# Kernel tuning notes

Measured on AMD Instinct MI355X. Metric: run time of the kernel, lower is better.

The kernel has to match this reference:

```python
import jax, jax.numpy as jnp
import numpy as np

K = 3
PAD = 1
DIL = 1
EPS = 1e-5


def _conv2d(x, w, b=None, pad=1):
    y = jax.lax.conv_general_dilated(x, w, (1, 1), [(pad, pad), (pad, pad)],
                                     dimension_numbers=('NCHW', 'OIHW', 'NCHW'))
    if b is not None:
        y = y + b[None, :, None, None]
    return y


def _conv_transpose(x, w, stride=2, pad=1):
    # torch ConvTranspose2d(k=4, s=2, p=1): lhs-dilated conv with flipped, transposed kernel
    kh = w.shape[2]
    w_t = jnp.flip(w, (2, 3)).transpose(1, 0, 2, 3)  # [in,out,kh,kw] -> [out,in,kh,kw]
    p = kh - 1 - pad
    return jax.lax.conv_general_dilated(x, w_t, (1, 1), [(p, p), (p, p)],
                                        lhs_dilation=(stride, stride),
                                        dimension_numbers=('NCHW', 'OIHW', 'NCHW'))


def _bn(x, g, b):
    # BatchNorm2d training-mode forward (batch stats, biased var)
    m = x.mean(axis=(0, 2, 3), keepdims=True)
    v = x.var(axis=(0, 2, 3), keepdims=True)
    return (x - m) * jax.lax.rsqrt(v + EPS) * g[None, :, None, None] + b[None, :, None, None]


def _deform_conv(x, off_x, off_y, mask, w):
    # Modulated deformable conv v2, stride=1, pad=K//2, groups=1, deform_groups=1
    B, C, H, W = x.shape
    K2 = K * K
    ky, kx = jnp.meshgrid(jnp.arange(K), jnp.arange(K), indexing='ij')
    base_y = (ky.reshape(-1) * DIL - PAD).astype(x.dtype)  # [K2]
    base_x = (kx.reshape(-1) * DIL - PAD).astype(x.dtype)
    hh = jnp.arange(H, dtype=x.dtype)
    ww = jnp.arange(W, dtype=x.dtype)
    # sampling coords per kernel tap: [B, K2, H, W]
    sy = off_y + base_y[None, :, None, None] + hh[None, None, :, None]
    sx = off_x + base_x[None, :, None, None] + ww[None, None, None, :]
    y0 = jnp.floor(sy)
    x0 = jnp.floor(sx)
    ly = sy - y0
    lx = sx - x0
    xf = x.reshape(B, C, H * W)

    def corner(yi, xi, wgt):
        valid = ((yi >= 0) & (yi < H) & (xi >= 0) & (xi < W)).astype(x.dtype)
        idx = (jnp.clip(yi, 0, H - 1) * W + jnp.clip(xi, 0, W - 1)).astype(jnp.int32)
        idx = idx.reshape(B, K2, H * W)
        v = jnp.take_along_axis(xf[:, :, None, :], idx[:, None, :, :], axis=3)  # [B,C,K2,HW]
        return v * (wgt * valid).reshape(B, 1, K2, H * W)

    val = (corner(y0, x0, (1 - ly) * (1 - lx)) + corner(y0, x0 + 1, (1 - ly) * lx)
           + corner(y0 + 1, x0, ly * (1 - lx)) + corner(y0 + 1, x0 + 1, ly * lx))
    val = val * mask.reshape(B, 1, K2, H * W)  # modulation
    O = w.shape[0]
    out = jnp.einsum('bip,oi->bop', val.reshape(B, C * K2, H * W), w.reshape(O, C * K2))
    return out.reshape(B, O, H, W)


def setup_inputs() -> dict:
    key = jax.random.key(0)
    ks = jax.random.split(key, 6)
    B, C, H, W, O = 4, 256, 64, 64, 256
    x = jax.random.normal(ks[0], (B, C, H, W), jnp.float32)
    w_off = jax.random.normal(ks[1], (3 * K * K, C, K, K), jnp.float32) * 0.01
    b_off = jax.random.normal(ks[2], (3 * K * K,), jnp.float32) * 0.01
    w_dcn = jax.random.normal(ks[3], (O, C, K, K), jnp.float32) * float(np.sqrt(2.0 / (C * K * K)))
    w_up = jax.random.normal(ks[4], (O, O, 4, 4), jnp.float32) * 0.02
    gamma1 = jnp.ones((O,), jnp.float32)
    beta1 = jnp.zeros((O,), jnp.float32)
    gamma2 = jnp.ones((O,), jnp.float32)
    beta2 = jnp.zeros((O,), jnp.float32)
    return dict(x=x, w_off=w_off, b_off=b_off, w_dcn=w_dcn, gamma1=gamma1, beta1=beta1,
                w_up=w_up, gamma2=gamma2, beta2=beta2)


def reference(x, w_off, b_off, w_dcn, gamma1, beta1, w_up, gamma2, beta2):
    offset_mask = _conv2d(x, w_off, b_off, pad=K // 2)
    off_x, off_y, mask = jnp.split(offset_mask, 3, axis=1)
    mask = jax.nn.sigmoid(mask)
    y = _deform_conv(x, off_x, off_y, mask, w_dcn)
    y = jax.nn.relu(_bn(y, gamma1, beta1))
    y_up = _conv_transpose(y, w_up)
    y_up = jax.nn.relu(_bn(y_up, gamma2, beta2))
    return (y, y_up)
```

## Files before the change

kernel.cpp:

```cpp
#include <hip/hip_runtime.h>
#include <math.h>

#define BB 4
#define CC 256
#define OC 256
#define HH 64
#define WW2 64
#define HW 4096
#define UP_HW 16384
#define NOFF 27
#define EPSV 1e-5f
#define TPX 32

typedef _Float16 f16;
typedef f16 f16x2 __attribute__((ext_vector_type(2)));
typedef f16 f16x4 __attribute__((ext_vector_type(4)));
typedef f16 f16x8 __attribute__((ext_vector_type(8)));
typedef float f32x4 __attribute__((ext_vector_type(4)));

#define GLOAD16(GP, LP) __builtin_amdgcn_global_load_lds( \
    (const __attribute__((address_space(1))) void*)(GP),  \
    (__attribute__((address_space(3))) void*)(LP), 16, 0, 0)

__global__ __launch_bounds__(256) void k_offset(
    const float* __restrict__ x, const float* __restrict__ w,
    const float* __restrict__ bias, float* __restrict__ om) {
  const int b = blockIdx.z;
  const int ocg = blockIdx.y * 3;
  const int row = threadIdx.x >> 6;
  const int h = blockIdx.x * 4 + row;
  const int col = threadIdx.x & 63;
  const float* xb = x + (size_t)b * CC * HW;
  float a0 = 0.f, a1 = 0.f, a2 = 0.f;
  for (int ic = 0; ic < CC; ++ic) {
    const float* xc = xb + ic * HW;
    float xm[3], xl[3], xr[3];
    #pragma unroll
    for (int dy = 0; dy < 3; ++dy) {
      int hy = h + dy - 1;
      float v = (hy >= 0 && hy < HH) ? xc[hy * WW2 + col] : 0.f;
      xm[dy] = v;
      float up = __shfl_up(v, 1, 64);
      float dn = __shfl_down(v, 1, 64);
      xl[dy] = (col == 0) ? 0.f : up;
      xr[dy] = (col == 63) ? 0.f : dn;
    }
    #pragma unroll
    for (int j = 0; j < 3; ++j) {
      const float* wp = w + ((size_t)(ocg + j) * CC + ic) * 9;
      float s = 0.f;
      #pragma unroll
      for (int dy = 0; dy < 3; ++dy) {
        s = fmaf(wp[dy * 3 + 0], xl[dy], s);
        s = fmaf(wp[dy * 3 + 1], xm[dy], s);
        s = fmaf(wp[dy * 3 + 2], xr[dy], s);
      }
      if (j == 0) a0 += s; else if (j == 1) a1 += s; else a2 += s;
    }
  }
  #pragma unroll
  for (int j = 0; j < 3; ++j) {
    int oc = ocg + j;
    float v = (j == 0 ? a0 : (j == 1 ? a1 : a2)) + bias[oc];
    if (oc >= 18) v = 1.f / (1.f + expf(-v));
    om[((size_t)(b * NOFF + oc)) * HW + h * WW2 + col] = v;
  }
}

__global__ __launch_bounds__(256) void k_dcn(
    const float* __restrict__ x, const float* __restrict__ om,
    const float* __restrict__ wd, float* __restrict__ out) {
  __shared__ int s_idx[4][TPX * 9];
  __shared__ float s_bw[4][TPX * 9];
  __shared__ __align__(16) float s_v[2][TPX * 9];
  __shared__ __align__(16) float s_wd[2][9][256];
  const int b = blockIdx.y;
  const int p0 = blockIdx.x * TPX;
  const int h = p0 >> 6;
  const int tid = threadIdx.x;

  for (int e = tid; e < TPX * 9; e += 256) {
    int px = e & (TPX - 1);
    int k = e >> 5;
    int p = p0 + px;
    int wc = p & 63;
    float offx = om[((size_t)(b * NOFF + k)) * HW + p];
    float offy = om[((size_t)(b * NOFF + 9 + k)) * HW + p];
    float msk  = om[((size_t)(b * NOFF + 18 + k)) * HW + p];
    float sy = offy + (float)(k / 3 - 1) + (float)h;
    float sx = offx + (float)(k % 3 - 1) + (float)wc;
    float fy = floorf(sy), fx = floorf(sx);
    float ly = sy - fy, lx = sx - fx;
    int iy = (int)fy, ix = (int)fx;
    #pragma unroll
    for (int cnr = 0; cnr < 4; ++cnr) {
      int dy = cnr >> 1, dx = cnr & 1;
      int yy = iy + dy, xx = ix + dx;
      bool val = (yy >= 0) & (yy < HH) & (xx >= 0) & (xx < WW2);
      float wt = (dy ? ly : 1.f - ly) * (dx ? lx : 1.f - lx) * msk;
      s_idx[cnr][e] = val ? (yy * WW2 + xx) : 0;
      s_bw[cnr][e] = val ? wt : 0.f;
    }
  }
  __syncthreads();

  const int og = tid >> 3, pg = tid & 7;
  float acc[8][4] = {};
  const float* xb = x + (size_t)b * CC * HW;
  for (int ic = 0; ic < CC; ic += 2) {
    {
      const float* wp = wd + (size_t)tid * (CC * 9) + ic * 9;
      #pragma unroll
      for (int t = 0; t < 18; ++t)
        s_wd[t / 9][t % 9][tid] = wp[t];
    }
    #pragma unroll
    for (int t = 0; t < 3; ++t) {
      int e = tid + t * 256;
      if (e < 2 * TPX * 9) {
        int icc = (e >= TPX * 9);
        int r = e - icc * TPX * 9;
        const float* xc = xb + (ic + icc) * HW;
        float v = s_bw[0][r] * xc[s_idx[0][r]] + s_bw[1][r] * xc[s_idx[1][r]]
                + s_bw[2][r] * xc[s_idx[2][r]] + s_bw[3][r] * xc[s_idx[3][r]];
        s_v[icc][r] = v;
      }
    }
    __syncthreads();
    #pragma unroll
    for (int icc = 0; icc < 2; ++icc) {
      #pragma unroll
      for (int k = 0; k < 9; ++k) {
        float4 v4 = *(const float4*)&s_v[icc][k * TPX + pg * 4];
        float4 wa = *(const float4*)&s_wd[icc][k][og * 8];
        float4 wb = *(const float4*)&s_wd[icc][k][og * 8 + 4];
        float vi[4] = {v4.x, v4.y, v4.z, v4.w};
        float wj[8] = {wa.x, wa.y, wa.z, wa.w, wb.x, wb.y, wb.z, wb.w};
        #pragma unroll
        for (int j = 0; j < 8; ++j)
          #pragma unroll
          for (int i = 0; i < 4; ++i)
            acc[j][i] = fmaf(wj[j], vi[i], acc[j][i]);
      }
    }
    __syncthreads();
  }
  #pragma unroll
  for (int j = 0; j < 8; ++j) {
    int oc = og * 8 + j;
    float4 o = make_float4(acc[j][0], acc[j][1], acc[j][2], acc[j][3]);
    *(float4*)&out[((size_t)(b * OC + oc)) * HW + p0 + pg * 4] = o;
  }
}

__global__ __launch_bounds__(256) void k_stats(
    const float* __restrict__ d, int perB, float* __restrict__ mean,
    float* __restrict__ rinv) {
  const int c = blockIdx.x, tid = threadIdx.x;
  double s1 = 0.0, s2 = 0.0;
  const int n4 = perB >> 2;
  for (int b = 0; b < BB; ++b) {
    const float4* p = (const float4*)(d + ((size_t)(b * CC + c)) * perB);
    for (int i = tid; i < n4; i += 256) {
      float4 v = p[i];
      s1 += (double)v.x + (double)v.y + (double)v.z + (double)v.w;
      s2 += (double)v.x * v.x + (double)v.y * v.y + (double)v.z * v.z + (double)v.w * v.w;
    }
  }
  __shared__ double r1[256], r2[256];
  r1[tid] = s1; r2[tid] = s2;
  __syncthreads();
  for (int s = 128; s > 0; s >>= 1) {
    if (tid < s) { r1[tid] += r1[tid + s]; r2[tid] += r2[tid + s]; }
    __syncthreads();
  }
  if (tid == 0) {
    double n = (double)perB * BB;
    double m = r1[0] / n;
    double var = r2[0] / n - m * m;
    mean[c] = (float)m;
    rinv[c] = (float)(1.0 / sqrt(var + (double)EPSV));
  }
}

__global__ __launch_bounds__(256) void k_stats_part(
    const float* __restrict__ d, int perB, double* __restrict__ part) {
  const int c = blockIdx.x & 255, b = blockIdx.x >> 8;
  const int tid = threadIdx.x;
  double s1 = 0.0, s2 = 0.0;
  const float4* p = (const float4*)(d + ((size_t)(b * CC + c)) * perB);
  const int n4 = perB >> 2;
  for (int i = tid; i < n4; i += 256) {
    float4 v = p[i];
    s1 += (double)v.x + (double)v.y + (double)v.z + (double)v.w;
    s2 += (double)v.x * v.x + (double)v.y * v.y + (double)v.z * v.z + (double)v.w * v.w;
  }
  __shared__ double r1[256], r2[256];
  r1[tid] = s1; r2[tid] = s2;
  __syncthreads();
  for (int s = 128; s > 0; s >>= 1) {
    if (tid < s) { r1[tid] += r1[tid + s]; r2[tid] += r2[tid + s]; }
    __syncthreads();
  }
  if (tid == 0) {
    part[blockIdx.x] = r1[0];
    part[1024 + blockIdx.x] = r2[0];
  }
}

__global__ __launch_bounds__(256) void k_stats_fin(
    const double* __restrict__ part, int perB, float* __restrict__ mean,
    float* __restrict__ rinv) {
  const int c = threadIdx.x;
  double s1 = 0.0, s2 = 0.0;
  #pragma unroll
  for (int b = 0; b < BB; ++b) {
    s1 += part[b * 256 + c];
    s2 += part[1024 + b * 256 + c];
  }
  double n = (double)perB * BB;
  double m = s1 / n;
  double var = s2 / n - m * m;
  mean[c] = (float)m;
  rinv[c] = (float)(1.0 / sqrt(var + (double)EPSV));
}

__global__ __launch_bounds__(256) void k_bnrelu(
    float* __restrict__ d, const float* __restrict__ mean,
    const float* __restrict__ rinv, const float* __restrict__ g,
    const float* __restrict__ be, int perB, int total4) {
  int stride = gridDim.x * blockDim.x;
  for (int i4 = blockIdx.x * blockDim.x + threadIdx.x; i4 < total4; i4 += stride) {
    int c = (int)((((long long)i4 * 4) / perB) & 255);
    float sc = rinv[c] * g[c];
    float shv = fmaf(-mean[c], sc, be[c]);
    float4 v = ((float4*)d)[i4];
    v.x = fmaxf(fmaf(v.x, sc, shv), 0.f);
    v.y = fmaxf(fmaf(v.y, sc, shv), 0.f);
    v.z = fmaxf(fmaf(v.z, sc, shv), 0.f);
    v.w = fmaxf(fmaf(v.w, sc, shv), 0.f);
    ((float4*)d)[i4] = v;
  }
}

__global__ __launch_bounds__(256) void k_totile(const float* __restrict__ y,
                                                f16* __restrict__ yTp) {
  __shared__ float S[32][33];
  const int h = blockIdx.x;
  const int cg = blockIdx.y >> 1;
  const int wg = blockIdx.y & 1;
  const int b = blockIdx.z;
  const int t = threadIdx.x;
  {
    int ci = t >> 3, q = t & 7;
    const float* src = y + (((size_t)(b * 256 + cg * 32 + ci) * 64 + h) * 64 + wg * 32 + q * 4);
    float4 v = *(const float4*)src;
    S[ci][q * 4 + 0] = v.x; S[ci][q * 4 + 1] = v.y;
    S[ci][q * 4 + 2] = v.z; S[ci][q * 4 + 3] = v.w;
  }
  __syncthreads();
  {
    int w = t >> 3, c2 = t & 7;
    f16x4 pv;
    pv[0] = (f16)S[c2 * 4 + 0][w];
    pv[1] = (f16)S[c2 * 4 + 1][w];
    pv[2] = (f16)S[c2 * 4 + 2][w];
    pv[3] = (f16)S[c2 * 4 + 3][w];
    f16* dst = yTp + (((size_t)(b * 66 + h + 1) * 66 + (wg * 32 + w + 1)) * 256 + cg * 32 + c2 * 4);
    *(f16x4*)dst = pv;
  }
}

__global__ __launch_bounds__(256) void k_totile_bn(
    const float* __restrict__ mean, const float* __restrict__ rinv,
    const float* __restrict__ g, const float* __restrict__ be,
    float* __restrict__ y, f16* __restrict__ yTp) {
  __shared__ float S[32][33];
  const int h = blockIdx.x;
  const int cg = blockIdx.y >> 1;
  const int wg = blockIdx.y & 1;
  const int b = blockIdx.z;
  const int t = threadIdx.x;
  {
    int ci = t >> 3, q = t & 7;
    int c = cg * 32 + ci;
    float sc = rinv[c] * g[c];
    float sh = fmaf(-mean[c], sc, be[c]);
    float* src = y + (((size_t)(b * 256 + c) * 64 + h) * 64 + wg * 32 + q * 4);
    float4 v = *(const float4*)src;
    v.x = fmaxf(fmaf(v.x, sc, sh), 0.f);
    v.y = fmaxf(fmaf(v.y, sc, sh), 0.f);
    v.z = fmaxf(fmaf(v.z, sc, sh), 0.f);
    v.w = fmaxf(fmaf(v.w, sc, sh), 0.f);
    *(float4*)src = v;
    S[ci][q * 4 + 0] = v.x; S[ci][q * 4 + 1] = v.y;
    S[ci][q * 4 + 2] = v.z; S[ci][q * 4 + 3] = v.w;
  }
  __syncthreads();
  {
    int w = t >> 3, c2 = t & 7;
    f16x4 pv;
    pv[0] = (f16)S[c2 * 4 + 0][w];
    pv[1] = (f16)S[c2 * 4 + 1][w];
    pv[2] = (f16)S[c2 * 4 + 2][w];
    pv[3] = (f16)S[c2 * 4 + 3][w];
    f16* dst = yTp + (((size_t)(b * 66 + h + 1) * 66 + (wg * 32 + w + 1)) * 256 + cg * 32 + c2 * 4);
    *(f16x4*)dst = pv;
  }
}

__global__ __launch_bounds__(128) void k_pad0(f16* __restrict__ p0,
                                              f16* __restrict__ p1) {
  f16* base = blockIdx.z ? p1 : p0;
  const int j = blockIdx.x;
  const int b = blockIdx.y;
  int row, col;
  if (j < 66)       { row = 0;      col = j; }
  else if (j < 132) { row = 65;     col = j - 66; }
  else if (j < 196) { row = j - 131; col = 0; }
  else              { row = j - 195; col = 65; }
  unsigned int* p = (unsigned int*)&base[(((size_t)b * 66 + row) * 66 + col) * 256];
  p[threadIdx.x] = 0u;
}

__global__ __launch_bounds__(256) void k_wdprep(const float* __restrict__ wd,
                                                f16* __restrict__ Wd) {
  const int oc = blockIdx.x, ic = threadIdx.x;
  const float* src = wd + ((size_t)oc * 256 + ic) * 9;
  f16* dst = Wd + (((size_t)(ic >> 3) * 256 + oc)) * 8 + (ic & 7);
  #pragma unroll
  for (int tap = 0; tap < 9; ++tap)
    dst[(size_t)tap * 32 * 256 * 8] = (f16)src[tap];
}

__global__ __launch_bounds__(256) void k_wodprep(const float* __restrict__ wo,
                                                 f16* __restrict__ Wod) {
  const int oc = blockIdx.x;
  const int ic = threadIdx.x;
  const int icg = ic >> 3, e = ic & 7;
  #pragma unroll
  for (int tap = 0; tap < 9; ++tap) {
    f16 v = (f16)0.f;
    if (oc < NOFF) v = (f16)wo[((size_t)oc * 256 + ic) * 9 + tap];
    Wod[(((size_t)(tap * 32 + icg)) * 32 + oc) * 8 + e] = v;
  }
}

__global__ __launch_bounds__(256) void k_off_mfma(
    const f16* __restrict__ xtp, const f16* __restrict__ Wod,
    const float* __restrict__ bias, float* __restrict__ om) {
  __shared__ __align__(16) f16 Alds[9 * 4 * 32 * 8];
  __shared__ __align__(16) f16 Blds[3 * 4 * 66 * 8];
  const int b = blockIdx.y;
  const int r = blockIdx.x;
  const int tid = threadIdx.x;
  const int lane = tid & 63, wave = tid >> 6;
  const int l15 = lane & 15, l4 = lane >> 4;
  const int wbase = tid & 192;
  f32x4 acc[2] = {};
  const size_t xbase = ((size_t)b * 66 + r) * 66;

  for (int ic0 = 0; ic0 < 256; ic0 += 32) {
    __syncthreads();
    #pragma unroll
    for (int i = 0; i < 5; ++i) {
      int idx = i * 256 + tid;
      if (idx < 1152) {
        int tap = idx >> 7, g = (idx >> 5) & 3, oc = idx & 31;
        const f16* gp = Wod + (((size_t)(tap * 32 + (ic0 >> 3) + g)) * 32 + oc) * 8;
        GLOAD16(gp, Alds + (size_t)(i * 256 + wbase) * 8);
      }
    }
    #pragma unroll
    for (int i = 0; i < 4; ++i) {
      int idx = i * 256 + tid;
      if (idx < 792) {
        int rp4g = idx / 66, c = idx - rp4g * 66;
        int rp = rp4g >> 2, g = rp4g & 3;
        const f16* gp = xtp + ((xbase + rp * 66 + c) * 256 + ic0 + g * 8);
        GLOAD16(gp, Blds + (size_t)(i * 256 + wbase) * 8);
      }
    }
    __syncthreads();
    #pragma unroll
    for (int tap = 0; tap < 9; ++tap) {
      const int ky = tap / 3, kx = tap % 3;
      f16x8 af[2];
      #pragma unroll
      for (int fi = 0; fi < 2; ++fi)
        af[fi] = *(const f16x8*)&Alds[((tap * 4 + l4) * 32 + fi * 16 + l15) * 8];
      f16x8 bf = *(const f16x8*)&Blds[((ky * 4 + l4) * 66 + wave * 16 + l15 + kx) * 8];
      #pragma unroll
      for (int fi = 0; fi < 2; ++fi)
        acc[fi] = __builtin_amdgcn_mfma_f32_16x16x32_f16(af[fi], bf, acc[fi], 0, 0, 0);
    }
  }
  #pragma unroll
  for (int fi = 0; fi < 2; ++fi) {
    #pragma unroll
    for (int r4 = 0; r4 < 4; ++r4) {
      int oc = fi * 16 + l4 * 4 + r4;
      if (oc < NOFF) {
        float v = acc[fi][r4] + bias[oc];
        if (oc >= 18) v = 1.f / (1.f + expf(-v));
        om[((size_t)(b * NOFF + oc)) * HW + r * 64 + wave * 16 + l15] = v;
      }
    }
  }
}

__global__ __launch_bounds__(256) void k_sample(
    const f16* __restrict__ xtp, const float* __restrict__ om,
    f16* __restrict__ V, int b0) {
  const int tap = blockIdx.y;
  const int vb = blockIdx.z;
  const int b = b0 + vb;
  const int p = blockIdx.x * 64 + (threadIdx.x & 63);
  const int icg0 = threadIdx.x >> 6;
  const int h = p >> 6, w = p & 63;
  const float offx = om[((size_t)(b * NOFF + tap)) * HW + p];
  const float offy = om[((size_t)(b * NOFF + 9 + tap)) * HW + p];
  const float msk  = om[((size_t)(b * NOFF + 18 + tap)) * HW + p];
  float sy = offy + (float)(tap / 3 - 1) + (float)h;
  float sx = offx + (float)(tap % 3 - 1) + (float)w;
  float fy = floorf(sy), fx = floorf(sx);
  float ly = sy - fy, lx = sx - fx;
  int iy = (int)fy, ix = (int)fx;
  int idx[4];
  float wg[4];
  #pragma unroll
  for (int cnr = 0; cnr < 4; ++cnr) {
    int dy = cnr >> 1, dx = cnr & 1;
    int yy = iy + dy, xx = ix + dx;
    bool val = (yy >= 0) & (yy < HH) & (xx >= 0) & (xx < WW2);
    float wt = (dy ? ly : 1.f - ly) * (dx ? lx : 1.f - lx) * msk;
    idx[cnr] = val ? ((yy + 1) * 66 + (xx + 1)) : 0;
    wg[cnr] = val ? wt : 0.f;
  }
  const f16* xb = xtp + (size_t)b * 66 * 66 * 256;
  f16* vout = V + (((size_t)(vb * 9 + tap) * 32) * HW + p) * 8;
  #pragma unroll
  for (int it = 0; it < 8; ++it) {
    int icg = icg0 + it * 4;
    f16x8 c0 = *(const f16x8*)(xb + (size_t)idx[0] * 256 + icg * 8);
    f16x8 c1 = *(const f16x8*)(xb + (size_t)idx[1] * 256 + icg * 8);
    f16x8 c2 = *(const f16x8*)(xb + (size_t)idx[2] * 256 + icg * 8);
    f16x8 c3 = *(const f16x8*)(xb + (size_t)idx[3] * 256 + icg * 8);
    f16x8 r;
    #pragma unroll
    for (int e = 0; e < 8; ++e) {
      float s = wg[0] * (float)c0[e];
      s = fmaf(wg[1], (float)c1[e], s);
      s = fmaf(wg[2], (float)c2[e], s);
      s = fmaf(wg[3], (float)c3[e], s);
      r[e] = (f16)s;
    }
    *(f16x8*)(vout + (size_t)icg * HW * 8) = r;
  }
}

__global__ __launch_bounds__(256) void k_dcn_mfma(
    const f16* __restrict__ V, const f16* __restrict__ Wd,
    float* __restrict__ out, int b0) {
  __shared__ __align__(16) f16 Alds[8 * 128 * 8];
  __shared__ __align__(16) f16 Blds[8 * 128 * 8];
  const int vb = blockIdx.z;
  const int b = b0 + vb;
  const int oc0 = blockIdx.y * 128;
  const int px0 = blockIdx.x * 128;
  const int tid = threadIdx.x;
  const int lane = tid & 63;
  const int wave = tid >> 6;
  const int wm = wave >> 1, wn = wave & 1;
  const int l15 = lane & 15, l4 = lane >> 4;
  const int wbase = tid & 192;
  f32x4 acc[4][4] = {};

  for (int tap = 0; tap < 9; ++tap) {
    for (int kk = 0; kk < 4; ++kk) {
      __syncthreads();
      #pragma unroll
      for (int i = 0; i < 4; ++i) {
        int idx = i * 256 + tid;
        int g = idx >> 7, q = idx & 127;
        const f16* gpA = Wd + (((size_t)((tap * 32 + kk * 8 + g) * 256) + oc0 + q)) * 8;
        const f16* gpB = V + ((((size_t)(vb * 9 + tap) * 32) + kk * 8 + g) * HW + px0 + q) * 8;
        f16* lpA = Alds + (size_t)(i * 256 + wbase) * 8;
        f16* lpB = Blds + (size_t)(i * 256 + wbase) * 8;
        GLOAD16(gpA, lpA);
        GLOAD16(gpB, lpB);
      }
      __syncthreads();
      #pragma unroll
      for (int half = 0; half < 2; ++half) {
        f16x8 af[4], bf[4];
        #pragma unroll
        for (int fi = 0; fi < 4; ++fi)
          af[fi] = *(const f16x8*)&Alds[(((half * 4 + l4) * 128) + wm * 64 + fi * 16 + l15) * 8];
        #pragma unroll
        for (int ni = 0; ni < 4; ++ni)
          bf[ni] = *(const f16x8*)&Blds[(((half * 4 + l4) * 128) + wn * 64 + ni * 16 + l15) * 8];
        #pragma unroll
        for (int fi = 0; fi < 4; ++fi)
          #pragma unroll
          for (int ni = 0; ni < 4; ++ni)
            acc[fi][ni] = __builtin_amdgcn_mfma_f32_16x16x32_f16(af[fi], bf[ni], acc[fi][ni], 0, 0, 0);
      }
    }
  }
  #pragma unroll
  for (int fi = 0; fi < 4; ++fi) {
    int oc = oc0 + wm * 64 + fi * 16 + l4 * 4;
    #pragma unroll
    for (int ni = 0; ni < 4; ++ni) {
      int px = px0 + wn * 64 + ni * 16 + l15;
      float* op = out + ((size_t)(b * OC + oc)) * HW + px;
      #pragma unroll
      for (int r = 0; r < 4; ++r)
        op[(size_t)r * HW] = acc[fi][ni][r];
    }
  }
}

__global__ __launch_bounds__(256) void k_wprep(const float* __restrict__ wu,
                                               f16* __restrict__ Wt) {
  const int ic = blockIdx.x * 2;
  const int oc = threadIdx.x;
  float a[16], c[16];
  const float* p0 = wu + ((size_t)(ic * 256 + oc)) * 16;
  const float* p1 = wu + ((size_t)((ic + 1) * 256 + oc)) * 16;
  #pragma unroll
  for (int k = 0; k < 4; ++k) {
    float4 v = *(const float4*)(p0 + k * 4);
    a[k * 4 + 0] = v.x; a[k * 4 + 1] = v.y; a[k * 4 + 2] = v.z; a[k * 4 + 3] = v.w;
    float4 w2 = *(const float4*)(p1 + k * 4);
    c[k * 4 + 0] = w2.x; c[k * 4 + 1] = w2.y; c[k * 4 + 2] = w2.z; c[k * 4 + 3] = w2.w;
  }
  #pragma unroll
  for (int kh = 0; kh < 4; ++kh)
    #pragma unroll
    for (int kw = 0; kw < 4; ++kw) {
      int po = (kh & 1) ^ 1, dh = kh >> 1;
      int qo = (kw & 1) ^ 1, dw = kw >> 1;
      int combo = (po * 2 + qo) * 4 + (dh * 2 + dw);
      f16x2 pv;
      pv[0] = (f16)a[kh * 4 + kw];
      pv[1] = (f16)c[kh * 4 + kw];
      *(f16x2*)&Wt[((size_t)(combo * 256 + oc)) * 256 + ic] = pv;
    }
}

__global__ __launch_bounds__(256) void k_up_mfma(
    const f16* __restrict__ yTp, const f16* __restrict__ Wt,
    float* __restrict__ out) {
  __shared__ __align__(16) f16 Alds[4 * 4 * 128 * 8];
  __shared__ __align__(16) f16 Blds[5 * 4 * 66 * 8];
  const int b = blockIdx.z;
  const int sub = blockIdx.y >> 1;
  const int po = sub >> 1, qo = sub & 1;
  const int oc0 = (blockIdx.y & 1) * 128;
  const int sh0 = blockIdx.x * 4;
  const int tid = threadIdx.x;
  const int lane = tid & 63, wave = tid >> 6;
  const int wm = wave >> 1, wn = wave & 1;
  const int l15 = lane & 15, l4 = lane >> 4;
  const int wbase = tid & 192;
  f32x4 acc[4][8] = {};
  const size_t yrow = ((size_t)b * 66 + (sh0 + po)) * 66;

  for (int ic0 = 0; ic0 < 256; ic0 += 32) {
    __syncthreads();
    #pragma unroll
    for (int i = 0; i < 8; ++i) {
      int idx = i * 256 + tid;
      int tap = idx >> 9, g = (idx >> 7) & 3, oc = idx & 127;
      const f16* gp = Wt + (((size_t)((sub * 4 + tap) * 256 + oc0 + oc)) * 256 + ic0 + g * 8);
      GLOAD16(gp, Alds + (size_t)(i * 256 + wbase) * 8);
    }
    #pragma unroll
    for (int i = 0; i < 6; ++i) {
      int idx = i * 256 + tid;
      if (idx < 1320) {
        int rp4g = idx / 66, c = idx - rp4g * 66;
        int rp = rp4g >> 2, g = rp4g & 3;
        const f16* gp = yTp + ((yrow + rp * 66 + c) * 256 + ic0 + g * 8);
        GLOAD16(gp, Blds + (size_t)(i * 256 + wbase) * 8);
      }
    }
    __syncthreads();
    #pragma unroll
    for (int tap = 0; tap < 4; ++tap) {
      const int dh = tap >> 1, dw = tap & 1;
      f16x8 af[4];
      #pragma unroll
      for (int fi = 0; fi < 4; ++fi)
        af[fi] = *(const f16x8*)&Alds[((tap * 4 + l4) * 128 + wm * 64 + fi * 16 + l15) * 8];
      #pragma unroll
      for (int ni = 0; ni < 8; ++ni) {
        int px = wn * 128 + ni * 16 + l15;
        int prow = px >> 6;
        int cp = (px & 63) + qo - dw + 1;
        f16x8 bf = *(const f16x8*)&Blds[(((prow + 1 - dh) * 4 + l4) * 66 + cp) * 8];
        #pragma unroll
        for (int fi = 0; fi < 4; ++fi)
          acc[fi][ni] = __builtin_amdgcn_mfma_f32_16x16x32_f16(af[fi], bf, acc[fi][ni], 0, 0, 0);
      }
    }
  }
  #pragma unroll
  for (int fi = 0; fi < 4; ++fi) {
    int oc = oc0 + wm * 64 + fi * 16 + l4 * 4;
    #pragma unroll
    for (int ni = 0; ni < 8; ++ni) {
      int px = wn * 128 + ni * 16 + l15;
      int sh = sh0 + (px >> 6);
      int ow = 2 * (px & 63) + qo;
      float* op = out + ((size_t)(b * 256 + oc)) * UP_HW + (2 * sh + po) * 128 + ow;
      #pragma unroll
      for (int r = 0; r < 4; ++r)
        op[(size_t)r * UP_HW] = acc[fi][ni][r];
    }
  }
}

extern "C" void kernel_launch(void* const* d_in, const int* in_sizes, int n_in,
                              void* d_out, int out_size, void* d_ws, size_t ws_size,
                              hipStream_t stream) {
  const float* x      = (const float*)d_in[0];
  const float* w_off  = (const float*)d_in[1];
  const float* b_off  = (const float*)d_in[2];
  const float* w_dcn  = (const float*)d_in[3];
  const float* gamma1 = (const float*)d_in[4];
  const float* beta1  = (const float*)d_in[5];
  const float* w_up   = (const float*)d_in[6];
  const float* gamma2 = (const float*)d_in[7];
  const float* beta2  = (const float*)d_in[8];

  float* out1 = (float*)d_out;
  float* out2 = out1 + (size_t)BB * OC * HW;

  char* wsb = (char*)d_ws;
  float* om    = (float*)wsb;
  float* mean1 = (float*)(wsb + 1769472);
  float* rinv1 = mean1 + 256;
  float* mean2 = rinv1 + 256;
  float* rinv2 = mean2 + 256;
  f16* yTp = (f16*)(wsb + 1773568);
  f16* Wt  = (f16*)(wsb + 10694656);
  f16* xtp = (f16*)(wsb + 12791808);
  f16* Wd  = (f16*)(wsb + 21712896);
  f16* Wod = (f16*)(wsb + 22892544);
  f16* V   = (f16*)(wsb + 23040000);
  const size_t FIXED_END = 23040000;
  const size_t VB_BYTES = 18874368;

  int nb = 0;
  if (ws_size >= FIXED_END + 4 * VB_BYTES) nb = 4;
  else if (ws_size >= FIXED_END + 2 * VB_BYTES) nb = 2;
  else if (ws_size >= FIXED_END + VB_BYTES) nb = 1;

  hipLaunchKernelGGL(k_wprep, dim3(128), dim3(256), 0, stream, w_up, Wt);

  if (nb > 0) {
    double* partd = (double*)V;
    hipLaunchKernelGGL(k_pad0, dim3(260, BB, 2), dim3(128), 0, stream, yTp, xtp);
    hipLaunchKernelGGL(k_totile, dim3(64, 16, BB), dim3(256), 0, stream, x, xtp);
    hipLaunchKernelGGL(k_wodprep, dim3(32), dim3(256), 0, stream, w_off, Wod);
    hipLaunchKernelGGL(k_wdprep, dim3(256), dim3(256), 0, stream, w_dcn, Wd);
    hipLaunchKernelGGL(k_off_mfma, dim3(64, BB), dim3(256), 0, stream, xtp, Wod, b_off, om);
    for (int b0 = 0; b0 < BB; b0 += nb) {
      hipLaunchKernelGGL(k_sample, dim3(64, 9, nb), dim3(256), 0, stream, xtp, om, V, b0);
      hipLaunchKernelGGL(k_dcn_mfma, dim3(32, 2, nb), dim3(256), 0, stream, V, Wd, out1, b0);
    }
    hipLaunchKernelGGL(k_stats_part, dim3(1024), dim3(256), 0, stream, out1, HW, partd);
    hipLaunchKernelGGL(k_stats_fin, dim3(1), dim3(256), 0, stream, partd, HW, mean1, rinv1);
    hipLaunchKernelGGL(k_totile_bn, dim3(64, 16, BB), dim3(256), 0, stream,
                       mean1, rinv1, gamma1, beta1, out1, yTp);
    hipLaunchKernelGGL(k_up_mfma, dim3(16, 8, BB), dim3(256), 0, stream, yTp, Wt, out2);
    hipLaunchKernelGGL(k_stats_part, dim3(1024), dim3(256), 0, stream, out2, UP_HW, partd);
    hipLaunchKernelGGL(k_stats_fin, dim3(1), dim3(256), 0, stream, partd, UP_HW, mean2, rinv2);
  } else {
    hipLaunchKernelGGL(k_pad0, dim3(260, BB, 1), dim3(128), 0, stream, yTp, yTp);
    hipLaunchKernelGGL(k_offset, dim3(16, 9, BB), dim3(256), 0, stream, x, w_off, b_off, om);
    hipLaunchKernelGGL(k_dcn, dim3(HW / TPX, BB), dim3(256), 0, stream, x, om, w_dcn, out1);
    hipLaunchKernelGGL(k_stats, dim3(256), dim3(256), 0, stream, out1, HW, mean1, rinv1);
    hipLaunchKernelGGL(k_bnrelu, dim3(2048), dim3(256), 0, stream, out1, mean1, rinv1,
                       gamma1, beta1, HW, (BB * OC * HW) / 4);
    hipLaunchKernelGGL(k_totile, dim3(64, 16, BB), dim3(256), 0, stream, out1, yTp);
    hipLaunchKernelGGL(k_up_mfma, dim3(16, 8, BB), dim3(256), 0, stream, yTp, Wt, out2);
    hipLaunchKernelGGL(k_stats, dim3(256), dim3(256), 0, stream, out2, UP_HW, mean2, rinv2);
  }

  hipLaunchKernelGGL(k_bnrelu, dim3(2048), dim3(256), 0, stream, out2, mean2, rinv2,
                     gamma2, beta2, UP_HW, (BB * OC * UP_HW) / 4);
}
```

Before: 213.2 us.

## Double-buffer LDS tiles in DCN and upsample MFMA GEMMs to overlap loads

```diff
diff --git a/kernel.cpp b/kernel.cpp
--- a/kernel.cpp
+++ b/kernel.cpp
@@ -459,11 +459,23 @@
   }
 }
 
+#define DCN_STAGE(BUF, S) { \
+    int tap_ = (S) >> 2, kk_ = (S) & 3; \
+    _Pragma("unroll") \
+    for (int i = 0; i < 4; ++i) { \
+      int idx = i * 256 + tid; \
+      int g = idx >> 7, q = idx & 127; \
+      const f16* gpA = Wd + (((size_t)((tap_ * 32 + kk_ * 8 + g) * 256) + oc0 + q)) * 8; \
+      const f16* gpB = V + ((vrow + tap_ * 32 + kk_ * 8 + g) * HW + px0 + q) * 8; \
+      GLOAD16(gpA, Alds[BUF] + (size_t)(i * 256 + wbase) * 8); \
+      GLOAD16(gpB, Blds[BUF] + (size_t)(i * 256 + wbase) * 8); \
+    } }
+
 __global__ __launch_bounds__(256) void k_dcn_mfma(
     const f16* __restrict__ V, const f16* __restrict__ Wd,
     float* __restrict__ out, int b0) {
-  __shared__ __align__(16) f16 Alds[8 * 128 * 8];
-  __shared__ __align__(16) f16 Blds[8 * 128 * 8];
+  __shared__ __align__(16) f16 Alds[2][8 * 128 * 8];
+  __shared__ __align__(16) f16 Blds[2][8 * 128 * 8];
   const int vb = blockIdx.z;
   const int b = b0 + vb;
   const int oc0 = blockIdx.y * 128;
@@ -475,38 +487,38 @@
   const int l15 = lane & 15, l4 = lane >> 4;
   const int wbase = tid & 192;
   f32x4 acc[4][4] = {};
-
-  for (int tap = 0; tap < 9; ++tap) {
-    for (int kk = 0; kk < 4; ++kk) {
-      __syncthreads();
-      #pragma unroll
-      for (int i = 0; i < 4; ++i) {
-        int idx = i * 256 + tid;
-        int g = idx >> 7, q = idx & 127;
-        const f16* gpA = Wd + (((size_t)((tap * 32 + kk * 8 + g) * 256) + oc0 + q)) * 8;
-        const f16* gpB = V + ((((size_t)(vb * 9 + tap) * 32) + kk * 8 + g) * HW + px0 + q) * 8;
-        f16* lpA = Alds + (size_t)(i * 256 + wbase) * 8;
-        f16* lpB = Blds + (size_t)(i * 256 + wbase) * 8;
-        GLOAD16(gpA, lpA);
-        GLOAD16(gpB, lpB);
-      }
-      __syncthreads();
-      #pragma unroll
-      for (int half = 0; half < 2; ++half) {
-        f16x8 af[4], bf[4];
-        #pragma unroll
-        for (int fi = 0; fi < 4; ++fi)
-          af[fi] = *(const f16x8*)&Alds[(((half * 4 + l4) * 128) + wm * 64 + fi * 16 + l15) * 8];
+  const size_t vrow = (size_t)(vb * 9) * 32;
+
+  DCN_STAGE(0, 0);
+  for (int s = 0; s < 36; ++s) {
+    const int cur = s & 1;
+    if (s < 35) {
+      DCN_STAGE(cur ^ 1, s + 1);
+      asm volatile("s_waitcnt vmcnt(8)" ::: "memory");
+    } else {
+      asm volatile("s_waitcnt vmcnt(0)" ::: "memory");
+    }
+    __builtin_amdgcn_s_barrier();
+    __builtin_amdgcn_sched_barrier(0);
+    asm volatile("" ::: "memory");
+    #pragma unroll
+    for (int half = 0; half < 2; ++half) {
+      f16x8 af[4], bf[4];
+      #pragma unroll
+      for (int fi = 0; fi < 4; ++fi)
+        af[fi] = *(const f16x8*)&Alds[cur][(((half * 4 + l4) * 128) + wm * 64 + fi * 16 + l15) * 8];
+      #pragma unroll
+      for (int ni = 0; ni < 4; ++ni)
+        bf[ni] = *(const f16x8*)&Blds[cur][(((half * 4 + l4) * 128) + wn * 64 + ni * 16 + l15) * 8];
+      #pragma unroll
+      for (int fi = 0; fi < 4; ++fi)
         #pragma unroll
         for (int ni = 0; ni < 4; ++ni)
-          bf[ni] = *(const f16x8*)&Blds[(((half * 4 + l4) * 128) + wn * 64 + ni * 16 + l15) * 8];
-        #pragma unroll
-        for (int fi = 0; fi < 4; ++fi)
-          #pragma unroll
-          for (int ni = 0; ni < 4; ++ni)
-            acc[fi][ni] = __builtin_amdgcn_mfma_f32_16x16x32_f16(af[fi], bf[ni], acc[fi][ni], 0, 0, 0);
-      }
-    }
+          acc[fi][ni] = __builtin_amdgcn_mfma_f32_16x16x32_f16(af[fi], bf[ni], acc[fi][ni], 0, 0, 0);
+    }
+    asm volatile("" ::: "memory");
+    __builtin_amdgcn_sched_barrier(0);
+    __builtin_amdgcn_s_barrier();
   }
   #pragma unroll
   for (int fi = 0; fi < 4; ++fi) {
@@ -550,11 +562,29 @@
     }
 }
 
+#define UP_STAGE(BUF, IC0) { \
+    _Pragma("unroll") \
+    for (int i = 0; i < 8; ++i) { \
+      int idx = i * 256 + tid; \
+      int tap = idx >> 9, g = (idx >> 7) & 3, oc = idx & 127; \
+      const f16* gp = Wt + (((size_t)((sub * 4 + tap) * 256 + oc0 + oc)) * 256 + (IC0) + g * 8); \
+      GLOAD16(gp, Alds[BUF] + (size_t)(i * 256 + wbase) * 8); \
+    } \
+    _Pragma("unroll") \
+    for (int i = 0; i < 6; ++i) { \
+      int idx = i * 256 + tid; \
+      int cidx = idx < 1320 ? idx : 1319; \
+      int rp4g = cidx / 66, c = cidx - rp4g * 66; \
+      int rp = rp4g >> 2, g = rp4g & 3; \
+      const f16* gp = yTp + ((yrow + rp * 66 + c) * 256 + (IC0) + g * 8); \
+      GLOAD16(gp, Blds[BUF] + (size_t)(i * 256 + wbase) * 8); \
+    } }
+
 __global__ __launch_bounds__(256) void k_up_mfma(
     const f16* __restrict__ yTp, const f16* __restrict__ Wt,
     float* __restrict__ out) {
-  __shared__ __align__(16) f16 Alds[4 * 4 * 128 * 8];
-  __shared__ __align__(16) f16 Blds[5 * 4 * 66 * 8];
+  __shared__ __align__(16) f16 Alds[2][4 * 4 * 128 * 8];
+  __shared__ __align__(16) f16 Blds[2][6 * 256 * 8];
   const int b = blockIdx.z;
   const int sub = blockIdx.y >> 1;
   const int po = sub >> 1, qo = sub & 1;
@@ -568,44 +598,39 @@
   f32x4 acc[4][8] = {};
   const size_t yrow = ((size_t)b * 66 + (sh0 + po)) * 66;
 
-  for (int ic0 = 0; ic0 < 256; ic0 += 32) {
-    __syncthreads();
-    #pragma unroll
-    for (int i = 0; i < 8; ++i) {
-      int idx = i * 256 + tid;
-      int tap = idx >> 9, g = (idx >> 7) & 3, oc = idx & 127;
-      const f16* gp = Wt + (((size_t)((sub * 4 + tap) * 256 + oc0 + oc)) * 256 + ic0 + g * 8);
-      GLOAD16(gp, Alds + (size_t)(i * 256 + wbase) * 8);
-    }
-    #pragma unroll
-    for (int i = 0; i < 6; ++i) {
-      int idx = i * 256 + tid;
-      if (idx < 1320) {
-        int rp4g = idx / 66, c = idx - rp4g * 66;
-        int rp = rp4g >> 2, g = rp4g & 3;
-        const f16* gp = yTp + ((yrow + rp * 66 + c) * 256 + ic0 + g * 8);
-        GLOAD16(gp, Blds + (size_t)(i * 256 + wbase) * 8);
-      }
-    }
-    __syncthreads();
+  UP_STAGE(0, 0);
+  for (int s = 0; s < 8; ++s) {
+    const int cur = s & 1;
+    if (s < 7) {
+      UP_STAGE(cur ^ 1, (s + 1) * 32);
+      asm volatile("s_waitcnt vmcnt(14)" ::: "memory");
+    } else {
+      asm volatile("s_waitcnt vmcnt(0)" ::: "memory");
+    }
+    __builtin_amdgcn_s_barrier();
+    __builtin_amdgcn_sched_barrier(0);
+    asm volatile("" ::: "memory");
     #pragma unroll
     for (int tap = 0; tap < 4; ++tap) {
       const int dh = tap >> 1, dw = tap & 1;
       f16x8 af[4];
       #pragma unroll
       for (int fi = 0; fi < 4; ++fi)
-        af[fi] = *(const f16x8*)&Alds[((tap * 4 + l4) * 128 + wm * 64 + fi * 16 + l15) * 8];
+        af[fi] = *(const f16x8*)&Alds[cur][((tap * 4 + l4) * 128 + wm * 64 + fi * 16 + l15) * 8];
       #pragma unroll
       for (int ni = 0; ni < 8; ++ni) {
         int px = wn * 128 + ni * 16 + l15;
         int prow = px >> 6;
         int cp = (px & 63) + qo - dw + 1;
-        f16x8 bf = *(const f16x8*)&Blds[(((prow + 1 - dh) * 4 + l4) * 66 + cp) * 8];
+        f16x8 bf = *(const f16x8*)&Blds[cur][(((prow + 1 - dh) * 4 + l4) * 66 + cp) * 8];
         #pragma unroll
         for (int fi = 0; fi < 4; ++fi)
           acc[fi][ni] = __builtin_amdgcn_mfma_f32_16x16x32_f16(af[fi], bf, acc[fi][ni], 0, 0, 0);
       }
     }
+    asm volatile("" ::: "memory");
+    __builtin_amdgcn_sched_barrier(0);
+    __builtin_amdgcn_s_barrier();
   }
   #pragma unroll
   for (int fi = 0; fi < 4; ++fi) {
```

New measurement: 237.1 us. 11.2% more time.
